# Kernel tuning notes

Hardware: AMD Instinct MI355X
Metric: run time of the kernel (lower is better)

The kernel has to match this reference:

```python
import jax, jax.numpy as jnp
import numpy as np

N, H, B = 1048576, 128, 4096


def setup_inputs() -> dict:
    key = jax.random.key(0)
    ks = jax.random.split(key, 10)
    x = jax.random.normal(ks[0], (N, H), dtype=jnp.float32)
    # sorted segment ids with every segment nonempty (matches torch.bincount/split usage)
    batch = jnp.sort(jnp.concatenate([
        jnp.arange(B, dtype=jnp.int32),
        jax.random.randint(ks[1], (N - B,), 0, B, dtype=jnp.int32),
    ]))
    s = 1.0 / np.sqrt(H)
    u = lambda k, shp: jax.random.uniform(k, shp, jnp.float32, -s, s)
    return {
        'session_embedding': x,
        'batch': batch,
        'W1': u(ks[2], (H, H)), 'b1': u(ks[3], (H,)),
        'W2': u(ks[4], (H, H)), 'b2': u(ks[5], (H,)),
        'Wq': u(ks[6], (1, H)), 'bq': u(ks[7], (1,)),
        'W3': u(ks[8], (H, 2 * H)), 'b3': u(ks[9], (H,)),
    }


def reference(session_embedding, batch, W1, b1, W2, b2, Wq, bq, W3, b3):
    # index of the last node in each session (batch is sorted)
    last_idx = jax.ops.segment_max(jnp.arange(N, dtype=jnp.int32), batch, num_segments=B)  # [B]
    v_n = session_embedding[last_idx]                      # [B, H]
    v_n_rep = v_n[batch]                                   # [N, H] last-node broadcast per node
    # attention logits: q(sigmoid(W1 v_n + W2 v_i))
    gate = jax.nn.sigmoid(v_n_rep @ W1.T + b1 + session_embedding @ W2.T + b2)  # [N, H]
    alpha = gate @ Wq.T + bq                               # [N, 1]
    s_g = jax.ops.segment_sum(alpha * session_embedding, batch, num_segments=B)  # [B, H]
    s_h = jnp.concatenate([v_n, s_g], axis=1) @ W3.T + b3  # [B, H]
    return s_h
```

## Files before the change

### kernel.cpp

```cpp
#include <hip/hip_runtime.h>
#include <hip/hip_bf16.h>

#define N_NODES 1048576
#define H 128
#define B_SESS 4096
#define TILE 64

typedef __attribute__((ext_vector_type(8))) short bf16x8;
typedef __attribute__((ext_vector_type(4))) short bf16x4;
typedef __attribute__((ext_vector_type(4))) float f32x4;

__device__ inline short bc(float f) {
  return (short)__builtin_bit_cast(unsigned short, __float2bfloat16(f));
}

__global__ void k_prep(const int* __restrict__ batch, int* __restrict__ last_idx,
                       const float* __restrict__ W2, unsigned short* __restrict__ W2b,
                       float* __restrict__ s_g) {
  int i = blockIdx.x * 256 + threadIdx.x;
  if (i < N_NODES) {
    if (i == N_NODES - 1 || batch[i] != batch[i + 1]) last_idx[batch[i]] = i;
  }
  if (i < B_SESS * H) s_g[i] = 0.f;
  if (i < 4096) {
    float4 v = *reinterpret_cast<const float4*>(W2 + (size_t)i * 4);
    bf16x4 o;
    o[0] = bc(v.x); o[1] = bc(v.y); o[2] = bc(v.z); o[3] = bc(v.w);
    *reinterpret_cast<bf16x4*>(W2b + (size_t)i * 4) = o;
  }
}

__global__ void k_apre(const float* __restrict__ x, const int* __restrict__ last_idx,
                       const float* __restrict__ W1, const float* __restrict__ b1,
                       const float* __restrict__ b2, float* __restrict__ A_pre) {
  __shared__ float Wl[128][132];
  __shared__ float vn[8][128];
  int t = threadIdx.x;
  for (int i = 0; i < 16; ++i) {
    int e = (t + i * 256) * 4;
    int r = e >> 7, c = e & 127;
    float4 v = *reinterpret_cast<const float4*>(W1 + e);
    Wl[r][c] = v.x; Wl[r][c + 1] = v.y; Wl[r][c + 2] = v.z; Wl[r][c + 3] = v.w;
  }
  int b0 = blockIdx.x * 8;
  for (int i = t; i < 8 * 128; i += 256) {
    int s = i >> 7, c = i & 127;
    vn[s][c] = x[(size_t)last_idx[b0 + s] * H + c];
  }
  __syncthreads();
  int h = t & 127, si = t >> 7;
  float bias = b1[h] + b2[h];
  for (int s = si; s < 8; s += 2) {
    float acc = bias;
    #pragma unroll
    for (int k = 0; k < 128; k += 4) {
      float4 w = *reinterpret_cast<const float4*>(&Wl[h][k]);
      acc += vn[s][k] * w.x + vn[s][k + 1] * w.y + vn[s][k + 2] * w.z + vn[s][k + 3] * w.w;
    }
    A_pre[(size_t)(b0 + s) * H + h] = acc;
  }
}

__global__ __launch_bounds__(256, 5)
void k_main(const float* __restrict__ x, const int* __restrict__ batch,
            const unsigned short* __restrict__ W2b, const float* __restrict__ Wq,
            const float* __restrict__ bq, const float* __restrict__ A_pre,
            float* __restrict__ s_g) {
  __shared__ unsigned short Wl[128][72];
  __shared__ float apre_s[16][128];
  __shared__ float alph[TILE];
  __shared__ int bsegs[TILE + 1];
  __shared__ float wqs[128];
  int t = threadIdx.x;
  int node0 = blockIdx.x * TILE;
  int w = t >> 6, lane = t & 63, r = lane & 15, ks = lane >> 4;
  int myrow = w * 16 + r;

  float4 af[8];
  const float* xrow = x + (size_t)(node0 + myrow) * H;
  #pragma unroll
  for (int k = 0; k < 4; ++k) {
    af[2 * k]     = *reinterpret_cast<const float4*>(xrow + k * 32 + ks * 8);
    af[2 * k + 1] = *reinterpret_cast<const float4*>(xrow + k * 32 + ks * 8 + 4);
  }
  bf16x8 w0[4], w1[4];
  #pragma unroll
  for (int i = 0; i < 4; ++i) {
    int u = t + i * 256, row = u >> 3, c = (u & 7) * 8;
    w0[i] = *reinterpret_cast<const bf16x8*>(W2b + row * 128 + c);
    w1[i] = *reinterpret_cast<const bf16x8*>(W2b + row * 128 + 64 + c);
  }
  int smin = batch[node0];
  int smax = batch[node0 + TILE - 1];
  int cnt = smax - smin + 1;
  bool fast = (cnt <= 16);
  if (fast) {
    const float4* src = reinterpret_cast<const float4*>(A_pre + ((size_t)smin << 7));
    float4* dst = reinterpret_cast<float4*>(&apre_s[0][0]);
    for (int i = t; i < cnt * 32; i += 256) dst[i] = src[i];
  }
  if (t <= TILE) {
    int idx = node0 + t;
    bsegs[t] = (idx < N_NODES) ? batch[idx] : -1;
  }
  if (t < 128) wqs[t] = Wq[t];
  #pragma unroll
  for (int i = 0; i < 4; ++i) {
    int u = t + i * 256, row = u >> 3, c = (u & 7) * 8;
    *reinterpret_cast<bf16x8*>(&Wl[row][c]) = w0[i];
  }
  bf16x8 afr[4];
  #pragma unroll
  for (int k = 0; k < 4; ++k) {
    float4 lo = af[2 * k], hi = af[2 * k + 1];
    bf16x8 v;
    v[0] = bc(lo.x); v[1] = bc(lo.y); v[2] = bc(lo.z); v[3] = bc(lo.w);
    v[4] = bc(hi.x); v[5] = bc(hi.y); v[6] = bc(hi.z); v[7] = bc(hi.w);
    afr[k] = v;
  }
  __syncthreads();

  f32x4 acc[8];
  #pragma unroll
  for (int nt = 0; nt < 8; ++nt) acc[nt] = (f32x4){0.f, 0.f, 0.f, 0.f};
  #pragma unroll
  for (int kg = 0; kg < 2; ++kg) {
    #pragma unroll
    for (int nt = 0; nt < 8; ++nt) {
      bf16x8 b = *reinterpret_cast<const bf16x8*>(&Wl[nt * 16 + r][kg * 32 + ks * 8]);
      acc[nt] = __builtin_amdgcn_mfma_f32_16x16x32_bf16(afr[kg], b, acc[nt], 0, 0, 0);
    }
  }
  __syncthreads();
  #pragma unroll
  for (int i = 0; i < 4; ++i) {
    int u = t + i * 256, row = u >> 3, c = (u & 7) * 8;
    *reinterpret_cast<bf16x8*>(&Wl[row][c]) = w1[i];
  }
  __syncthreads();
  #pragma unroll
  for (int kg = 2; kg < 4; ++kg) {
    #pragma unroll
    for (int nt = 0; nt < 8; ++nt) {
      bf16x8 b = *reinterpret_cast<const bf16x8*>(&Wl[nt * 16 + r][(kg - 2) * 32 + ks * 8]);
      acc[nt] = __builtin_amdgcn_mfma_f32_16x16x32_bf16(afr[kg], b, acc[nt], 0, 0, 0);
    }
  }

  int h = t & 127, grp = t >> 7;
  int base = grp * 32;
  const float* xp = x + (size_t)(node0 + base) * H + h;
  float xv[32];
  #pragma unroll
  for (int n = 0; n < 32; ++n) xv[n] = xp[(size_t)n * H];

  float bqv = bq[0];
  float pa[4];
#define DO_ALPHA(GET) do {                                                   \
    _Pragma("unroll")                                                        \
    for (int j = 0; j < 4; ++j) {                                            \
      int row = bsegs[w * 16 + ks * 4 + j];                                  \
      float s = 0.f;                                                         \
      _Pragma("unroll")                                                      \
      for (int nt = 0; nt < 8; ++nt) {                                       \
        int col = nt * 16 + r;                                               \
        float z = acc[nt][j] + (GET);                                        \
        float g = 1.0f / (1.0f + __expf(-z));                                \
        s += g * wqs[col];                                                   \
      }                                                                      \
      s += __shfl_xor(s, 1); s += __shfl_xor(s, 2);                          \
      s += __shfl_xor(s, 4); s += __shfl_xor(s, 8);                          \
      pa[j] = s + bqv;                                                       \
    } } while (0)
  if (fast) DO_ALPHA(apre_s[row - smin][col]);
  else      DO_ALPHA(A_pre[(size_t)row * H + col]);
#undef DO_ALPHA
  if (r == 0) {
    #pragma unroll
    for (int j = 0; j < 4; ++j) alph[w * 16 + ks * 4 + j] = pa[j];
  }
  __syncthreads();

  float accum = 0.f;
  #pragma unroll
  for (int n = 0; n < 32; ++n) {
    int ln = base + n;
    accum += alph[ln] * xv[n];
    if (bsegs[ln] != bsegs[ln + 1]) {
      atomicAdd(&s_g[(size_t)bsegs[ln] * H + h], accum);
      accum = 0.f;
    }
  }
  if (accum != 0.f) atomicAdd(&s_g[(size_t)bsegs[base + 31] * H + h], accum);
}

__global__ void k_final(const float* __restrict__ x, const int* __restrict__ last_idx,
                        const float* __restrict__ s_g, const float* __restrict__ W3,
                        const float* __restrict__ b3, float* __restrict__ out) {
  __shared__ float Wl[128][132];
  __shared__ float vin[8][256];
  int t = threadIdx.x;
  int b0 = blockIdx.x * 8;
  for (int i = t; i < 8 * 256; i += 256) {
    int s = i >> 8, c = i & 255;
    float v;
    if (c < 128) v = x[(size_t)last_idx[b0 + s] * H + c];
    else         v = s_g[(size_t)(b0 + s) * H + (c - 128)];
    vin[s][c] = v;
  }
  int h = t & 127, si = t >> 7;
  float res[4];
  for (int half = 0; half < 2; ++half) {
    __syncthreads();
    for (int i = 0; i < 16; ++i) {
      int e = (t + i * 256) * 4;
      int r = e >> 7, c = e & 127;
      float4 v = *reinterpret_cast<const float4*>(W3 + (size_t)r * 256 + half * 128 + c);
      Wl[r][c] = v.x; Wl[r][c + 1] = v.y; Wl[r][c + 2] = v.z; Wl[r][c + 3] = v.w;
    }
    __syncthreads();
    #pragma unroll
    for (int sI = 0; sI < 4; ++sI) {
      int s = si + sI * 2;
      float acc = 0.f;
      #pragma unroll
      for (int k = 0; k < 128; k += 4) {
        float4 wv = *reinterpret_cast<const float4*>(&Wl[h][k]);
        acc += vin[s][half * 128 + k] * wv.x + vin[s][half * 128 + k + 1] * wv.y +
               vin[s][half * 128 + k + 2] * wv.z + vin[s][half * 128 + k + 3] * wv.w;
      }
      if (half == 0) res[sI] = acc;
      else out[(size_t)(b0 + s) * H + h] = res[sI] + acc + b3[h];
    }
  }
}

extern "C" void kernel_launch(void* const* d_in, const int* in_sizes, int n_in,
                              void* d_out, int out_size, void* d_ws, size_t ws_size,
                              hipStream_t stream) {
  const float* x     = (const float*)d_in[0];
  const int*   batch = (const int*)d_in[1];
  const float* W1    = (const float*)d_in[2];
  const float* b1    = (const float*)d_in[3];
  const float* W2    = (const float*)d_in[4];
  const float* b2    = (const float*)d_in[5];
  const float* Wq    = (const float*)d_in[6];
  const float* bq    = (const float*)d_in[7];
  const float* W3    = (const float*)d_in[8];
  const float* b3    = (const float*)d_in[9];
  float* out = (float*)d_out;

  char* ws = (char*)d_ws;
  int*            last_idx = (int*)ws;
  float*          A_pre    = (float*)(ws + 16384);
  float*          s_g      = (float*)(ws + 16384 + 2097152);
  unsigned short* W2b      = (unsigned short*)(ws + 16384 + 2 * 2097152);

  k_prep<<<N_NODES / 256, 256, 0, stream>>>(batch, last_idx, W2, W2b, s_g);
  k_apre<<<B_SESS / 8, 256, 0, stream>>>(x, last_idx, W1, b1, b2, A_pre);
  k_main<<<N_NODES / TILE, 256, 0, stream>>>(x, batch, W2b, Wq, bq, A_pre, s_g);
  k_final<<<B_SESS / 8, 256, 0, stream>>>(x, last_idx, s_g, W3, b3, out);
}
```

Measured before the change: 214.9 us.

## Load full swizzled bf16 W2 into LDS via direct global-to-LDS loads

The prep kernel now writes W2 in bf16 with an XOR swizzle of 16-byte chunks per row. The main kernel loads the whole 32KB matrix straight into LDS with global_load_lds, replacing two register-staged halves and the extra barriers between them. The MFMA loop now runs all four k-groups in one pass using swizzled addresses to avoid bank conflicts, and the strided x column loads move after the alpha computation. The larger LDS footprint forces occupancy down to 4 blocks, and the A_pre fast-path cache shrinks to 8 sessions, so more tiles fall back to global A_pre reads.

```diff
diff --git a/kernel.cpp b/kernel.cpp
--- a/kernel.cpp
+++ b/kernel.cpp
@@ -15,18 +15,23 @@
 }
 
 __global__ void k_prep(const int* __restrict__ batch, int* __restrict__ last_idx,
-                       const float* __restrict__ W2, unsigned short* __restrict__ W2b,
+                       const float* __restrict__ W2, unsigned short* __restrict__ W2s,
                        float* __restrict__ s_g) {
   int i = blockIdx.x * 256 + threadIdx.x;
   if (i < N_NODES) {
     if (i == N_NODES - 1 || batch[i] != batch[i + 1]) last_idx[batch[i]] = i;
   }
   if (i < B_SESS * H) s_g[i] = 0.f;
-  if (i < 4096) {
-    float4 v = *reinterpret_cast<const float4*>(W2 + (size_t)i * 4);
-    bf16x4 o;
-    o[0] = bc(v.x); o[1] = bc(v.y); o[2] = bc(v.z); o[3] = bc(v.w);
-    *reinterpret_cast<bf16x4*>(W2b + (size_t)i * 4) = o;
+  if (i < 2048) {
+    int row = i >> 4, u = i & 15;
+    const float* src = W2 + row * 128 + u * 8;
+    float4 a = *reinterpret_cast<const float4*>(src);
+    float4 b = *reinterpret_cast<const float4*>(src + 4);
+    bf16x8 o;
+    o[0] = bc(a.x); o[1] = bc(a.y); o[2] = bc(a.z); o[3] = bc(a.w);
+    o[4] = bc(b.x); o[5] = bc(b.y); o[6] = bc(b.z); o[7] = bc(b.w);
+    int up = u ^ (row & 7);
+    *reinterpret_cast<bf16x8*>(W2s + row * 128 + up * 8) = o;
   }
 }
 
@@ -61,39 +66,42 @@
   }
 }
 
-__global__ __launch_bounds__(256, 5)
+__global__ __launch_bounds__(256, 4)
 void k_main(const float* __restrict__ x, const int* __restrict__ batch,
-            const unsigned short* __restrict__ W2b, const float* __restrict__ Wq,
+            const unsigned short* __restrict__ W2s, const float* __restrict__ Wq,
             const float* __restrict__ bq, const float* __restrict__ A_pre,
             float* __restrict__ s_g) {
-  __shared__ unsigned short Wl[128][72];
-  __shared__ float apre_s[16][128];
+  __shared__ unsigned short Wl[128][128];
+  __shared__ float apre_s[8][128];
   __shared__ float alph[TILE];
   __shared__ int bsegs[TILE + 1];
   __shared__ float wqs[128];
   int t = threadIdx.x;
   int node0 = blockIdx.x * TILE;
   int w = t >> 6, lane = t & 63, r = lane & 15, ks = lane >> 4;
-  int myrow = w * 16 + r;
+
+  #pragma unroll
+  for (int i = 0; i < 8; ++i) {
+    int seg = w * 8 + i;
+    __builtin_amdgcn_global_load_lds(
+        reinterpret_cast<const unsigned int*>(
+            reinterpret_cast<const char*>(W2s) + seg * 1024 + lane * 16),
+        reinterpret_cast<unsigned int*>(
+            reinterpret_cast<char*>(&Wl[0][0]) + seg * 1024),
+        16, 0, 0);
+  }
 
   float4 af[8];
-  const float* xrow = x + (size_t)(node0 + myrow) * H;
+  const float* xrow = x + (size_t)(node0 + w * 16 + r) * H;
   #pragma unroll
   for (int k = 0; k < 4; ++k) {
     af[2 * k]     = *reinterpret_cast<const float4*>(xrow + k * 32 + ks * 8);
     af[2 * k + 1] = *reinterpret_cast<const float4*>(xrow + k * 32 + ks * 8 + 4);
   }
-  bf16x8 w0[4], w1[4];
-  #pragma unroll
-  for (int i = 0; i < 4; ++i) {
-    int u = t + i * 256, row = u >> 3, c = (u & 7) * 8;
-    w0[i] = *reinterpret_cast<const bf16x8*>(W2b + row * 128 + c);
-    w1[i] = *reinterpret_cast<const bf16x8*>(W2b + row * 128 + 64 + c);
-  }
   int smin = batch[node0];
   int smax = batch[node0 + TILE - 1];
   int cnt = smax - smin + 1;
-  bool fast = (cnt <= 16);
+  bool fast = (cnt <= 8);
   if (fast) {
     const float4* src = reinterpret_cast<const float4*>(A_pre + ((size_t)smin << 7));
     float4* dst = reinterpret_cast<float4*>(&apre_s[0][0]);
@@ -104,55 +112,31 @@
     bsegs[t] = (idx < N_NODES) ? batch[idx] : -1;
   }
   if (t < 128) wqs[t] = Wq[t];
-  #pragma unroll
-  for (int i = 0; i < 4; ++i) {
-    int u = t + i * 256, row = u >> 3, c = (u & 7) * 8;
-    *reinterpret_cast<bf16x8*>(&Wl[row][c]) = w0[i];
-  }
+
   bf16x8 afr[4];
   #pragma unroll
-  for (int k = 0; k < 4; ++k) {
-    float4 lo = af[2 * k], hi = af[2 * k + 1];
+  for (int kg = 0; kg < 4; ++kg) {
+    const float* afp = reinterpret_cast<const float*>(af);
     bf16x8 v;
-    v[0] = bc(lo.x); v[1] = bc(lo.y); v[2] = bc(lo.z); v[3] = bc(lo.w);
-    v[4] = bc(hi.x); v[5] = bc(hi.y); v[6] = bc(hi.z); v[7] = bc(hi.w);
-    afr[k] = v;
+    #pragma unroll
+    for (int c = 0; c < 8; ++c) v[c] = bc(afp[kg * 8 + c]);
+    afr[kg] = v;
   }
   __syncthreads();
 
+  int sw = r & 7;
   f32x4 acc[8];
   #pragma unroll
   for (int nt = 0; nt < 8; ++nt) acc[nt] = (f32x4){0.f, 0.f, 0.f, 0.f};
   #pragma unroll
-  for (int kg = 0; kg < 2; ++kg) {
+  for (int kg = 0; kg < 4; ++kg) {
+    int up = (kg * 4 + ks) ^ sw;
     #pragma unroll
     for (int nt = 0; nt < 8; ++nt) {
-      bf16x8 b = *reinterpret_cast<const bf16x8*>(&Wl[nt * 16 + r][kg * 32 + ks * 8]);
+      bf16x8 b = *reinterpret_cast<const bf16x8*>(&Wl[nt * 16 + r][up * 8]);
       acc[nt] = __builtin_amdgcn_mfma_f32_16x16x32_bf16(afr[kg], b, acc[nt], 0, 0, 0);
     }
   }
-  __syncthreads();
-  #pragma unroll
-  for (int i = 0; i < 4; ++i) {
-    int u = t + i * 256, row = u >> 3, c = (u & 7) * 8;
-    *reinterpret_cast<bf16x8*>(&Wl[row][c]) = w1[i];
-  }
-  __syncthreads();
-  #pragma unroll
-  for (int kg = 2; kg < 4; ++kg) {
-    #pragma unroll
-    for (int nt = 0; nt < 8; ++nt) {
-      bf16x8 b = *reinterpret_cast<const bf16x8*>(&Wl[nt * 16 + r][(kg - 2) * 32 + ks * 8]);
-      acc[nt] = __builtin_amdgcn_mfma_f32_16x16x32_bf16(afr[kg], b, acc[nt], 0, 0, 0);
-    }
-  }
-
-  int h = t & 127, grp = t >> 7;
-  int base = grp * 32;
-  const float* xp = x + (size_t)(node0 + base) * H + h;
-  float xv[32];
-  #pragma unroll
-  for (int n = 0; n < 32; ++n) xv[n] = xp[(size_t)n * H];
 
   float bqv = bq[0];
   float pa[4];
@@ -179,6 +163,13 @@
     #pragma unroll
     for (int j = 0; j < 4; ++j) alph[w * 16 + ks * 4 + j] = pa[j];
   }
+
+  int h = t & 127, grp = t >> 7;
+  int base = grp * 32;
+  const float* xp = x + (size_t)(node0 + base) * H + h;
+  float xv[32];
+  #pragma unroll
+  for (int n = 0; n < 32; ++n) xv[n] = xp[(size_t)n * H];
   __syncthreads();
 
   float accum = 0.f;
@@ -187,11 +178,11 @@
     int ln = base + n;
     accum += alph[ln] * xv[n];
     if (bsegs[ln] != bsegs[ln + 1]) {
-      atomicAdd(&s_g[(size_t)bsegs[ln] * H + h], accum);
+      atomicAdd(&s_g[((size_t)bsegs[ln] << 7) + h], accum);
       accum = 0.f;
     }
   }
-  if (accum != 0.f) atomicAdd(&s_g[(size_t)bsegs[base + 31] * H + h], accum);
+  if (accum != 0.f) atomicAdd(&s_g[((size_t)bsegs[base + 31] << 7) + h], accum);
 }
 
 __global__ void k_final(const float* __restrict__ x, const int* __restrict__ last_idx,
@@ -254,10 +245,10 @@
   int*            last_idx = (int*)ws;
   float*          A_pre    = (float*)(ws + 16384);
   float*          s_g      = (float*)(ws + 16384 + 2097152);
-  unsigned short* W2b      = (unsigned short*)(ws + 16384 + 2 * 2097152);
-
-  k_prep<<<N_NODES / 256, 256, 0, stream>>>(batch, last_idx, W2, W2b, s_g);
+  unsigned short* W2s      = (unsigned short*)(ws + 16384 + 2 * 2097152);
+
+  k_prep<<<N_NODES / 256, 256, 0, stream>>>(batch, last_idx, W2, W2s, s_g);
   k_apre<<<B_SESS / 8, 256, 0, stream>>>(x, last_idx, W1, b1, b2, A_pre);
-  k_main<<<N_NODES / TILE, 256, 0, stream>>>(x, batch, W2b, Wq, bq, A_pre, s_g);
+  k_main<<<N_NODES / TILE, 256, 0, stream>>>(x, batch, W2s, Wq, bq, A_pre, s_g);
   k_final<<<B_SESS / 8, 256, 0, stream>>>(x, last_idx, s_g, W3, b3, out);
 }
```

Result: slower. 220.9 us (+2.8%).
